# Optimization experiments

Hardware: AMD Instinct MI355X
Metric: run time of the kernel (lower is better)

Reference implementation:

```python
import jax, jax.numpy as jnp
import numpy as np

B, F, P, H1, H2 = 4096, 1024, 64, 256, 128

def setup_inputs() -> dict:
    key = jax.random.key(0)
    ks = jax.random.split(key, 7)
    def glorot(k, shape, fan_in):
        bound = 1.0 / np.sqrt(fan_in)
        return jax.random.uniform(k, shape, jnp.float32, -bound, bound)
    return {
        "features": jax.random.normal(ks[0], (B, F), jnp.float32),
        "W1": glorot(ks[1], (P, F, H1), F),   # stacked per-predicate first-layer weights
        "b1": glorot(ks[2], (P, H1), F),
        "W2": glorot(ks[3], (P, H1, H2), H1),
        "b2": glorot(ks[4], (P, H2), H1),
        "W3": glorot(ks[5], (P, H2), H2),     # last layer out_dim=1, squeezed
        "b3": glorot(ks[6], (P,), H2),
    }

def reference(features, W1, b1, W2, b2, W3, b3):
    # All n_predicates MLPs as batched GEMMs (dropout = identity at inference).
    h1 = jax.nn.relu(jnp.einsum('bf,pfh->pbh', features, W1) + b1[:, None, :])  # [P,B,H1]
    h2 = jax.nn.relu(jnp.einsum('pbh,phk->pbk', h1, W2) + b2[:, None, :])       # [P,B,H2]
    logits = jnp.einsum('pbk,pk->pb', h2, W3) + b3[:, None]                      # [P,B]
    return jax.nn.sigmoid(logits).T  # [B, P] matching torch.cat(dim=1)
```

## Files before the change

kernel.cpp:

```cpp
#include <hip/hip_runtime.h>
#include <hip/hip_bf16.h>

#define B_SZ 4096
#define F_SZ 1024
#define P_SZ 64
#define H1D  256
#define H2D  128

typedef __attribute__((ext_vector_type(8))) short  short8;
typedef __attribute__((ext_vector_type(4))) float  floatx4;
typedef __attribute__((ext_vector_type(2))) float  float2v;
typedef __attribute__((ext_vector_type(4))) float  float4v;

typedef __attribute__((address_space(1))) const void* gas_t;
typedef __attribute__((address_space(3))) void*       las_t;

__device__ __forceinline__ short bfbits(float f) {
  __bf16 h = (__bf16)f;
  return __builtin_bit_cast(short, h);
}

__device__ __forceinline__ void gll16(const void* g, void* l) {
  __builtin_amdgcn_global_load_lds((gas_t)g, (las_t)l, 16, 0, 0);
}

#define WS_A_OFF   0
#define WS_W1_OFF  8388608UL
#define WS_W2_OFF  41943040UL
#define WS_NEEDED  46137344UL

__global__ __launch_bounds__(256) void prep_A(const float* __restrict__ feat,
                                              short8* __restrict__ outv) {
  const int c = blockIdx.x * 256 + threadIdx.x;
  const int row = c & 15, kg = (c >> 4) & 3, f = (c >> 6) & 7, kt = (c >> 9) & 31, mt = c >> 14;
  const float* src = feat + (size_t)(mt * 128 + f * 16 + row) * F_SZ + kt * 32 + kg * 8;
  float4v v0 = *(const float4v*)src;
  float4v v1 = *(const float4v*)(src + 4);
  short8 o;
  #pragma unroll
  for (int j = 0; j < 4; ++j) { o[j] = bfbits(v0[j]); o[4 + j] = bfbits(v1[j]); }
  outv[c] = o;
}

__global__ __launch_bounds__(256) void prep_W1(const float* __restrict__ W1,
                                               short8* __restrict__ outv) {
  const int c = blockIdx.x * 256 + threadIdx.x;
  const int nr = c & 15, kg = (c >> 4) & 3, nf = (c >> 6) & 15, kt = (c >> 10) & 31, p = c >> 15;
  const float* src = W1 + ((size_t)p * F_SZ + kt * 32 + kg * 8) * H1D + nf * 16 + nr;
  short8 o;
  #pragma unroll
  for (int j = 0; j < 8; ++j) o[j] = bfbits(src[(size_t)j * H1D]);
  outv[c] = o;
}

__global__ __launch_bounds__(256) void prep_W2(const float* __restrict__ W2,
                                               short8* __restrict__ outv) {
  const int c = blockIdx.x * 256 + threadIdx.x;
  const int qr = c & 15, kgl = (c >> 4) & 3, ks = (c >> 6) & 1, qf = (c >> 7) & 7,
            kc = (c >> 10) & 3, p = c >> 12;
  const float* src = W2 + ((size_t)p * H1D + kc * 64 + ks * 32 + kgl * 8) * H2D + qf * 16 + qr;
  short8 o;
  #pragma unroll
  for (int j = 0; j < 8; ++j) o[j] = bfbits(src[(size_t)j * H2D]);
  outv[c] = o;
}

__global__ __launch_bounds__(512, 2)
void fused_mlp_v5(const char* __restrict__ ws,
                  const float* __restrict__ b1,
                  const float* __restrict__ b2,
                  const float* __restrict__ W3,
                  const float* __restrict__ b3,
                  float* __restrict__ out) {
  __shared__ __align__(16) char sm[135168];

  const int tid  = threadIdx.x;
  const int lane = tid & 63;
  const int wid  = tid >> 6;
  const int wm   = wid >> 2;
  const int wn   = wid & 3;

  const int bid = blockIdx.x;
  const int wg  = (bid & 7) * 128 + (bid >> 3);
  const int p   = wg >> 4;
  const int mt  = wg & 15;
  const int m0  = mt * 256;

  const char* Apre  = ws + WS_A_OFF  + (size_t)(2 * mt) * 262144;
  const char* W1pre = ws + WS_W1_OFF + (size_t)p * 524288;
  const char* W2pre = ws + WS_W2_OFF + (size_t)p * 65536;

  floatx4 acc[8][4];
  #pragma unroll
  for (int i = 0; i < 8; ++i)
    #pragma unroll
    for (int j = 0; j < 4; ++j)
      acc[i][j] = (floatx4)0.0f;

  auto stage = [&](int ib, int kt) {
    char* base = sm + ib * 32768;
    gll16(Apre + (size_t)kt * 8192 + tid * 16,          base + wid * 1024);
    gll16(Apre + 262144 + (size_t)kt * 8192 + tid * 16, base + 8192 + wid * 1024);
    const char* gb = W1pre + (size_t)kt * 16384 + tid * 16;
    gll16(gb,        base + 16384 + wid * 1024);
    gll16(gb + 8192, base + 24576 + wid * 1024);
  };

  stage(0, 0);
  stage(1, 1);
  asm volatile("s_waitcnt vmcnt(4)" ::: "memory");
  __builtin_amdgcn_s_barrier();

  int ibr = 0;
  for (int t = 0; t < 32; ++t) {
    short8 af[8], bfr[4];
    #pragma unroll
    for (int mi = 0; mi < 8; ++mi)
      af[mi] = *(const short8*)(sm + ibr * 32768 + (wm * 8 + mi) * 1024 + lane * 16);
    #pragma unroll
    for (int ni = 0; ni < 4; ++ni)
      bfr[ni] = *(const short8*)(sm + ibr * 32768 + 16384 + (wn * 4 + ni) * 1024 + lane * 16);

    const int ibs = (ibr == 0) ? 2 : ibr - 1;
    if (t < 30) {
      stage(ibs, t + 2);
    } else {
      const int j0 = (t - 30) * 4;
      #pragma unroll
      for (int j = 0; j < 4; ++j)
        gll16(W2pre + (size_t)(j0 + j) * 8192 + tid * 16,
              sm + 65536 + (j0 + j) * 8192 + wid * 1024);
    }

    __builtin_amdgcn_s_setprio(1);
    #pragma unroll
    for (int mi = 0; mi < 8; ++mi)
      #pragma unroll
      for (int ni = 0; ni < 4; ++ni)
        acc[mi][ni] = __builtin_amdgcn_mfma_f32_16x16x32_bf16(af[mi], bfr[ni], acc[mi][ni], 0, 0, 0);
    __builtin_amdgcn_s_setprio(0);

    if (t < 31) {
      asm volatile("s_waitcnt vmcnt(4)" ::: "memory");
      __builtin_amdgcn_s_barrier();
    }
    ibr = (ibr == 2) ? 0 : ibr + 1;
  }
  __syncthreads();

  float b1v[4];
  #pragma unroll
  for (int ni = 0; ni < 4; ++ni)
    b1v[ni] = b1[p * H1D + wn * 64 + ni * 16 + (lane & 15)];

  floatx4 acc2[8][2];
  #pragma unroll
  for (int mi = 0; mi < 8; ++mi)
    #pragma unroll
    for (int qi = 0; qi < 2; ++qi)
      acc2[mi][qi] = (floatx4)0.0f;

  const int c  = lane & 15;
  const int hi = lane >> 4;

  #pragma unroll
  for (int h = 0; h < 2; ++h) {
    #pragma unroll
    for (int mi = 0; mi < 8; ++mi)
      #pragma unroll
      for (int ii = 0; ii < 2; ++ii) {
        const int ni  = h * 2 + ii;
        const int kg2 = ii * 2 + (c >> 3);
        const int base = (wn * 16 + wm * 8 + mi) * 1024 + kg2 * 256 + (c & 7) * 2;
        #pragma unroll
        for (int r = 0; r < 4; ++r) {
          const float v = fmaxf(acc[mi][ni][r] + b1v[ni], 0.0f);
          *(short*)(sm + base + (hi * 4 + r) * 16) = bfbits(v);
        }
      }
    __syncthreads();

    #pragma unroll
    for (int s = 0; s < 4; ++s) {
      short8 hf[8], wf[2];
      #pragma unroll
      for (int mi = 0; mi < 8; ++mi)
        hf[mi] = *(const short8*)(sm + (s * 16 + wm * 8 + mi) * 1024 + lane * 16);
      #pragma unroll
      for (int qi = 0; qi < 2; ++qi)
        wf[qi] = *(const short8*)(sm + 65536 + s * 16384 + (wn * 2 + qi) * 2048
                                  + h * 1024 + lane * 16);
      #pragma unroll
      for (int mi = 0; mi < 8; ++mi)
        #pragma unroll
        for (int qi = 0; qi < 2; ++qi)
          acc2[mi][qi] = __builtin_amdgcn_mfma_f32_16x16x32_bf16(hf[mi], wf[qi], acc2[mi][qi], 0, 0, 0);
    }
    __syncthreads();
  }

  float lsum[8][4];
  #pragma unroll
  for (int mi = 0; mi < 8; ++mi)
    #pragma unroll
    for (int r = 0; r < 4; ++r) lsum[mi][r] = 0.0f;

  #pragma unroll
  for (int qi = 0; qi < 2; ++qi) {
    const int q = wn * 32 + qi * 16 + c;
    const float b2v = b2[p * H2D + q];
    const float w3v = W3[p * H2D + q];
    #pragma unroll
    for (int mi = 0; mi < 8; ++mi)
      #pragma unroll
      for (int r = 0; r < 4; ++r) {
        const float h2v = fmaxf(acc2[mi][qi][r] + b2v, 0.0f);
        lsum[mi][r] += h2v * w3v;
      }
  }
  #pragma unroll
  for (int mask = 1; mask <= 8; mask <<= 1)
    #pragma unroll
    for (int mi = 0; mi < 8; ++mi)
      #pragma unroll
      for (int r = 0; r < 4; ++r)
        lsum[mi][r] += __shfl_xor(lsum[mi][r], mask, 64);

  float* part = (float*)(sm + 131072);
  if (c == 0) {
    #pragma unroll
    for (int mi = 0; mi < 8; ++mi)
      #pragma unroll
      for (int r = 0; r < 4; ++r)
        part[wn * 256 + wm * 128 + mi * 16 + hi * 4 + r] = lsum[mi][r];
  }
  __syncthreads();
  if (tid < 256) {
    const float x = part[tid] + part[256 + tid] + part[512 + tid] + part[768 + tid] + b3[p];
    const float s = 1.0f / (1.0f + __expf(-x));
    out[(size_t)(m0 + tid) * P_SZ + p] = s;
  }
}

__global__ __launch_bounds__(512, 2)
void fused_mlp_kernel(const float* __restrict__ feat,
                      const float* __restrict__ W1,
                      const float* __restrict__ b1,
                      const float* __restrict__ W2,
                      const float* __restrict__ b2,
                      const float* __restrict__ W3,
                      const float* __restrict__ b3,
                      float* __restrict__ out) {
  __shared__ __align__(16) char sm[49152];
  const int tid  = threadIdx.x;
  const int lane = tid & 63;
  const int wid  = tid >> 6;
  const int wm   = wid >> 2;
  const int wn   = wid & 3;
  const int bid = blockIdx.x;
  const int wg  = (bid & 7) * 256 + (bid >> 3);
  const int p   = wg >> 5;
  const int mt  = wg & 31;
  const int m0  = mt * 128;

  const float* featm = feat + (size_t)m0 * F_SZ;
  const float* W1p   = W1 + (size_t)p * F_SZ * H1D;
  const float* b1p   = b1 + p * H1D;
  const float* W2p   = W2 + (size_t)p * H1D * H2D;
  const float* b2p   = b2 + p * H2D;
  const float* W3p   = W3 + p * H2D;

  const int a_m  = tid >> 2;
  const int a_kg = tid & 3;
  const int b_n2 = tid & 127;
  const int b_kq = tid >> 7;

  float a_reg[8];
  float b_reg[16];
  floatx4 acc[4][4];
  #pragma unroll
  for (int i = 0; i < 4; ++i)
    #pragma unroll
    for (int j = 0; j < 4; ++j)
      acc[i][j] = (floatx4)0.0f;

  auto stage_load = [&](int k0) {
    const float* pa = featm + a_m * F_SZ + k0 + a_kg * 8;
    *(float4v*)(&a_reg[0]) = *(const float4v*)(pa);
    *(float4v*)(&a_reg[4]) = *(const float4v*)(pa + 4);
    #pragma unroll
    for (int i = 0; i < 8; ++i) {
      const float* pb = W1p + (size_t)(k0 + b_kq * 8 + i) * H1D + b_n2 * 2;
      *(float2v*)(&b_reg[2 * i]) = *(const float2v*)(pb);
    }
  };
  auto stage_write = [&](int cur) {
    short8 av;
    #pragma unroll
    for (int i = 0; i < 8; ++i) av[i] = bfbits(a_reg[i]);
    const int aslot = (a_m >> 4) * 64 + (a_m & 15) + a_kg * 16;
    *(short8*)(sm + cur * 8192 + aslot * 16) = av;
    #pragma unroll
    for (int dn = 0; dn < 2; ++dn) {
      short8 bv;
      #pragma unroll
      for (int i = 0; i < 8; ++i) bv[i] = bfbits(b_reg[2 * i + dn]);
      const int n = b_n2 * 2 + dn;
      const int bslot = (n >> 4) * 64 + (n & 15) + b_kq * 16;
      *(short8*)(sm + 16384 + cur * 16384 + bslot * 16) = bv;
    }
  };
  auto compute = [&](int cur) {
    short8 af[4], bfr[4];
    #pragma unroll
    for (int mi = 0; mi < 4; ++mi)
      af[mi] = *(const short8*)(sm + cur * 8192 + ((wm * 4 + mi) * 64 + lane) * 16);
    #pragma unroll
    for (int ni = 0; ni < 4; ++ni)
      bfr[ni] = *(const short8*)(sm + 16384 + cur * 16384 + ((wn * 4 + ni) * 64 + lane) * 16);
    #pragma unroll
    for (int mi = 0; mi < 4; ++mi)
      #pragma unroll
      for (int ni = 0; ni < 4; ++ni)
        acc[mi][ni] = __builtin_amdgcn_mfma_f32_16x16x32_bf16(af[mi], bfr[ni], acc[mi][ni], 0, 0, 0);
  };

  stage_load(0);
  stage_write(0);
  __syncthreads();
  int cur = 0;
  for (int t = 0; t < 32; ++t) {
    if (t + 1 < 32) stage_load((t + 1) * 32);
    compute(cur);
    if (t + 1 < 32) stage_write(cur ^ 1);
    __syncthreads();
    cur ^= 1;
  }

  floatx4 acc2[4][2];
  #pragma unroll
  for (int mi = 0; mi < 4; ++mi)
    #pragma unroll
    for (int qi = 0; qi < 2; ++qi)
      acc2[mi][qi] = (floatx4)0.0f;

  float b1v[4];
  #pragma unroll
  for (int ni = 0; ni < 4; ++ni)
    b1v[ni] = b1p[wn * 64 + ni * 16 + (lane & 15)];

  const int w2_q2 = tid & 63;
  const int w2_kq = tid >> 6;

  for (int kc = 0; kc < 4; ++kc) {
    const int kbase = kc * 64;
    float w2reg[16];
    #pragma unroll
    for (int i = 0; i < 8; ++i) {
      const float* pw = W2p + (size_t)(kbase + w2_kq * 8 + i) * H2D + w2_q2 * 2;
      *(float2v*)(&w2reg[2 * i]) = *(const float2v*)(pw);
    }
    #pragma unroll
    for (int dq = 0; dq < 2; ++dq) {
      short8 wv;
      #pragma unroll
      for (int i = 0; i < 8; ++i) wv[i] = bfbits(w2reg[2 * i + dq]);
      const int q = w2_q2 * 2 + dq;
      const int slot = ((q >> 4) * 2 + (w2_kq >> 2)) * 64 + (w2_kq & 3) * 16 + (q & 15);
      *(short8*)(sm + 16384 + slot * 16) = wv;
    }
    if (wn == kc) {
      #pragma unroll
      for (int mi = 0; mi < 4; ++mi) {
        #pragma unroll
        for (int ni = 0; ni < 4; ++ni) {
          const int kl = ni * 16 + (lane & 15);
          const int base = (((wm * 4 + mi) * 2 + (kl >> 5)) * 64 + ((kl >> 3) & 3) * 16) * 16
                           + (kl & 7) * 2;
          #pragma unroll
          for (int r = 0; r < 4; ++r) {
            float v = fmaxf(acc[mi][ni][r] + b1v[ni], 0.0f);
            const int row = (lane >> 4) * 4 + r;
            *(short*)(sm + base + row * 16) = bfbits(v);
          }
        }
      }
    }
    __syncthreads();
    #pragma unroll
    for (int ks = 0; ks < 2; ++ks) {
      short8 hf[4], wf[2];
      #pragma unroll
      for (int mi = 0; mi < 4; ++mi)
        hf[mi] = *(const short8*)(sm + (((wm * 4 + mi) * 2 + ks) * 64 + lane) * 16);
      #pragma unroll
      for (int qi = 0; qi < 2; ++qi)
        wf[qi] = *(const short8*)(sm + 16384 + (((wn * 2 + qi) * 2 + ks) * 64 + lane) * 16);
      #pragma unroll
      for (int mi = 0; mi < 4; ++mi)
        #pragma unroll
        for (int qi = 0; qi < 2; ++qi)
          acc2[mi][qi] = __builtin_amdgcn_mfma_f32_16x16x32_bf16(hf[mi], wf[qi], acc2[mi][qi], 0, 0, 0);
    }
    __syncthreads();
  }

  float lsum[4][4];
  #pragma unroll
  for (int mi = 0; mi < 4; ++mi)
    #pragma unroll
    for (int r = 0; r < 4; ++r) lsum[mi][r] = 0.0f;

  #pragma unroll
  for (int qi = 0; qi < 2; ++qi) {
    const int q = wn * 32 + qi * 16 + (lane & 15);
    const float b2v = b2p[q];
    const float w3v = W3p[q];
    #pragma unroll
    for (int mi = 0; mi < 4; ++mi)
      #pragma unroll
      for (int r = 0; r < 4; ++r) {
        const float h = fmaxf(acc2[mi][qi][r] + b2v, 0.0f);
        lsum[mi][r] += h * w3v;
      }
  }
  #pragma unroll
  for (int mask = 1; mask <= 8; mask <<= 1)
    #pragma unroll
    for (int mi = 0; mi < 4; ++mi)
      #pragma unroll
      for (int r = 0; r < 4; ++r)
        lsum[mi][r] += __shfl_xor(lsum[mi][r], mask, 64);

  float* part = (float*)(sm + 32768);
  if ((lane & 15) == 0) {
    const int g = lane >> 4;
    #pragma unroll
    for (int mi = 0; mi < 4; ++mi)
      #pragma unroll
      for (int r = 0; r < 4; ++r)
        part[wn * 128 + wm * 64 + mi * 16 + g * 4 + r] = lsum[mi][r];
  }
  __syncthreads();
  if (tid < 128) {
    const float x = part[tid] + part[128 + tid] + part[256 + tid] + part[384 + tid] + b3[p];
    const float s = 1.0f / (1.0f + __expf(-x));
    out[(size_t)(m0 + tid) * P_SZ + p] = s;
  }
}

extern "C" void kernel_launch(void* const* d_in, const int* in_sizes, int n_in,
                              void* d_out, int out_size, void* d_ws, size_t ws_size,
                              hipStream_t stream) {
  (void)in_sizes; (void)n_in; (void)out_size;
  const float* feat = (const float*)d_in[0];
  const float* W1   = (const float*)d_in[1];
  const float* b1   = (const float*)d_in[2];
  const float* W2   = (const float*)d_in[3];
  const float* b2   = (const float*)d_in[4];
  const float* W3   = (const float*)d_in[5];
  const float* b3   = (const float*)d_in[6];
  float* out = (float*)d_out;

  if (ws_size >= WS_NEEDED) {
    char* ws = (char*)d_ws;
    hipLaunchKernelGGL(prep_A,  dim3(2048), dim3(256), 0, stream, feat, (short8*)(ws + WS_A_OFF));
    hipLaunchKernelGGL(prep_W1, dim3(8192), dim3(256), 0, stream, W1,   (short8*)(ws + WS_W1_OFF));
    hipLaunchKernelGGL(prep_W2, dim3(1024), dim3(256), 0, stream, W2,   (short8*)(ws + WS_W2_OFF));
    hipLaunchKernelGGL(fused_mlp_v5, dim3(1024), dim3(512), 0, stream,
                       (const char*)ws, b1, b2, W3, b3, out);
  } else {
    hipLaunchKernelGGL(fused_mlp_kernel, dim3(2048), dim3(512), 0, stream,
                       feat, W1, b1, W2, b2, W3, b3, out);
  }
}
```

Measured before the change: 162.0 us.

## Split GEMM1 k-step into two half-phases interleaving LDS reads, loads and MFMAs

Each main-loop iteration of the first GEMM now runs as two phases: it reads half of the A fragments plus the B fragments, issues half of the next stage's global-to-LDS loads, and runs 16 MFMAs. Then it reads the remaining A fragments, issues the other half of the loads, and runs the remaining MFMAs. Extra barriers and sched_barriers pin this ordering so memory traffic interleaves with matrix work across the waves, in the style of a ping-pong schedule. The cost is more barriers per iteration and possible stalls from the tighter synchronisation.

Result: slower. 170.7 us (+5.4%).

```diff
diff --git a/kernel.cpp b/kernel.cpp
--- a/kernel.cpp
+++ b/kernel.cpp
@@ -66,7 +66,7 @@
 }
 
 __global__ __launch_bounds__(512, 2)
-void fused_mlp_v5(const char* __restrict__ ws,
+void fused_mlp_v6(const char* __restrict__ ws,
                   const float* __restrict__ b1,
                   const float* __restrict__ b2,
                   const float* __restrict__ W3,
@@ -105,6 +105,17 @@
     gll16(gb,        base + 16384 + wid * 1024);
     gll16(gb + 8192, base + 24576 + wid * 1024);
   };
+  auto stage_half = [&](int ib, int kt, int half) {
+    char* base = sm + ib * 32768;
+    if (half == 0) {
+      gll16(Apre + (size_t)kt * 8192 + tid * 16,          base + wid * 1024);
+      gll16(Apre + 262144 + (size_t)kt * 8192 + tid * 16, base + 8192 + wid * 1024);
+    } else {
+      const char* gb = W1pre + (size_t)kt * 16384 + tid * 16;
+      gll16(gb,        base + 16384 + wid * 1024);
+      gll16(gb + 8192, base + 24576 + wid * 1024);
+    }
+  };
 
   stage(0, 0);
   stage(1, 1);
@@ -113,35 +124,65 @@
 
   int ibr = 0;
   for (int t = 0; t < 32; ++t) {
-    short8 af[8], bfr[4];
-    #pragma unroll
-    for (int mi = 0; mi < 8; ++mi)
-      af[mi] = *(const short8*)(sm + ibr * 32768 + (wm * 8 + mi) * 1024 + lane * 16);
+    const char* rb  = sm + ibr * 32768;
+    const int   ibs = (ibr == 0) ? 2 : ibr - 1;
+
+    short8 af0[4], bfr[4];
+    #pragma unroll
+    for (int mi = 0; mi < 4; ++mi)
+      af0[mi] = *(const short8*)(rb + (wm * 8 + mi) * 1024 + lane * 16);
     #pragma unroll
     for (int ni = 0; ni < 4; ++ni)
-      bfr[ni] = *(const short8*)(sm + ibr * 32768 + 16384 + (wn * 4 + ni) * 1024 + lane * 16);
-
-    const int ibs = (ibr == 0) ? 2 : ibr - 1;
+      bfr[ni] = *(const short8*)(rb + 16384 + (wn * 4 + ni) * 1024 + lane * 16);
+
     if (t < 30) {
-      stage(ibs, t + 2);
+      stage_half(ibs, t + 2, 0);
     } else {
       const int j0 = (t - 30) * 4;
-      #pragma unroll
-      for (int j = 0; j < 4; ++j)
-        gll16(W2pre + (size_t)(j0 + j) * 8192 + tid * 16,
-              sm + 65536 + (j0 + j) * 8192 + wid * 1024);
-    }
-
+      gll16(W2pre + (size_t)j0 * 8192 + tid * 16,       sm + 65536 + j0 * 8192 + wid * 1024);
+      gll16(W2pre + (size_t)(j0 + 1) * 8192 + tid * 16, sm + 65536 + (j0 + 1) * 8192 + wid * 1024);
+    }
+
+    __builtin_amdgcn_s_barrier();
+    asm volatile("s_waitcnt lgkmcnt(0)" ::: "memory");
+    __builtin_amdgcn_sched_barrier(0);
     __builtin_amdgcn_s_setprio(1);
     #pragma unroll
-    for (int mi = 0; mi < 8; ++mi)
+    for (int mi = 0; mi < 4; ++mi)
       #pragma unroll
       for (int ni = 0; ni < 4; ++ni)
-        acc[mi][ni] = __builtin_amdgcn_mfma_f32_16x16x32_bf16(af[mi], bfr[ni], acc[mi][ni], 0, 0, 0);
+        acc[mi][ni] = __builtin_amdgcn_mfma_f32_16x16x32_bf16(af0[mi], bfr[ni], acc[mi][ni], 0, 0, 0);
+    __builtin_amdgcn_s_setprio(0);
+    __builtin_amdgcn_s_barrier();
+
+    short8 af1[4];
+    #pragma unroll
+    for (int mi = 0; mi < 4; ++mi)
+      af1[mi] = *(const short8*)(rb + (wm * 8 + 4 + mi) * 1024 + lane * 16);
+
+    if (t < 30) {
+      stage_half(ibs, t + 2, 1);
+    } else {
+      const int j0 = (t - 30) * 4 + 2;
+      gll16(W2pre + (size_t)j0 * 8192 + tid * 16,       sm + 65536 + j0 * 8192 + wid * 1024);
+      gll16(W2pre + (size_t)(j0 + 1) * 8192 + tid * 16, sm + 65536 + (j0 + 1) * 8192 + wid * 1024);
+    }
+
+    __builtin_amdgcn_s_barrier();
+    asm volatile("s_waitcnt lgkmcnt(0)" ::: "memory");
+    __builtin_amdgcn_sched_barrier(0);
+    __builtin_amdgcn_s_setprio(1);
+    #pragma unroll
+    for (int mi = 0; mi < 4; ++mi)
+      #pragma unroll
+      for (int ni = 0; ni < 4; ++ni)
+        acc[4 + mi][ni] = __builtin_amdgcn_mfma_f32_16x16x32_bf16(af1[mi], bfr[ni], acc[4 + mi][ni], 0, 0, 0);
     __builtin_amdgcn_s_setprio(0);
 
     if (t < 31) {
       asm volatile("s_waitcnt vmcnt(4)" ::: "memory");
+      __builtin_amdgcn_s_barrier();
+    } else {
       __builtin_amdgcn_s_barrier();
     }
     ibr = (ibr == 2) ? 0 : ibr + 1;
@@ -467,7 +508,7 @@
     hipLaunchKernelGGL(prep_A,  dim3(2048), dim3(256), 0, stream, feat, (short8*)(ws + WS_A_OFF));
     hipLaunchKernelGGL(prep_W1, dim3(8192), dim3(256), 0, stream, W1,   (short8*)(ws + WS_W1_OFF));
     hipLaunchKernelGGL(prep_W2, dim3(1024), dim3(256), 0, stream, W2,   (short8*)(ws + WS_W2_OFF));
-    hipLaunchKernelGGL(fused_mlp_v5, dim3(1024), dim3(512), 0, stream,
+    hipLaunchKernelGGL(fused_mlp_v6, dim3(1024), dim3(512), 0, stream,
                        (const char*)ws, b1, b2, W3, b3, out);
   } else {
     hipLaunchKernelGGL(fused_mlp_kernel, dim3(2048), dim3(512), 0, stream,
```
